# Performance work log

Measured on AMD Instinct MI355X. Metric: run time of the kernel, lower is better.

Reference implementation:

```python
import jax, jax.numpy as jnp
import numpy as np

N, E, F, C, H, DK, CV, RH, B, OUT = 50000, 800000, 32, 64, 4, 32, 16, 16, 128, 64


def setup_inputs() -> dict:
    key = jax.random.key(0)
    ks = jax.random.split(key, 16)
    s = lambda k, shape, fan: jax.random.normal(k, shape, jnp.float32) / np.float32(np.sqrt(fan))
    return {
        'pos': jax.random.normal(ks[0], (N, 3), jnp.float32),
        'node_features': jax.random.normal(ks[1], (N, F), jnp.float32),
        'edge_index': jax.random.randint(ks[2], (2, E), 0, N),
        'batch': jnp.sort(jax.random.randint(ks[3], (N,), 0, B)),
        'W_emb': s(ks[4], (F, C), F), 'b_emb': jnp.zeros((C,), jnp.float32),
        'Wq': s(ks[5], (H, C, DK), C), 'Wk': s(ks[6], (H, C, DK), C),
        'Wv0': s(ks[7], (H, C, CV), C), 'Wv1': s(ks[8], (H, C, CV), C),
        'R1': s(ks[9], (H, 1, RH), 1), 'b1': jnp.zeros((H, RH), jnp.float32),
        'R2': s(ks[10], (H, RH, DK + 2 * CV), RH), 'b2': jnp.zeros((H, DK + 2 * CV), jnp.float32),
        'Wproj': s(ks[11], (H * CV, OUT), H * CV),
    }


def reference(pos, node_features, edge_index, batch, W_emb, b_emb, Wq, Wk, Wv0, Wv1, R1, b1, R2, b2, Wproj):
    src, dst = edge_index[0], edge_index[1]
    # relative positions, distances, normalized directions (= l=1 spherical harmonics)
    rel = pos[dst] - pos[src]                       # [E,3]
    d = jnp.linalg.norm(rel, axis=-1, keepdims=True) + 1e-8  # [E,1]
    Y1 = rel / d                                    # l=1 SH (unit direction); l=0 SH is constant
    # initial scalar embedding (torch.nn.Linear)
    h = node_features @ W_emb + b_emb               # [N,C]
    hs = h[src]                                     # [E,C] edge gather
    # per-head queries / radially-modulated keys
    q = jnp.einsum('nc,hck->hnk', h, Wq)            # [H,N,DK]
    ksrc = jnp.einsum('ec,hck->hek', hs, Wk)        # [H,E,DK]
    rh = jax.nn.silu(jnp.einsum('ei,hir->her', d, R1) + b1[:, None, :])  # radial MLP [H,E,RH]
    rout = jnp.einsum('her,hro->heo', rh, R2) + b2[:, None, :]           # [H,E,DK+2CV]
    rk, rv0, rv1 = rout[..., :DK], rout[..., DK:DK + CV], rout[..., DK + CV:]
    ke = ksrc * rk
    scores = jnp.einsum('hek,hek->he', q[:, dst], ke).T / np.float32(np.sqrt(DK))  # [E,H]
    # segment softmax over incoming edges of each destination node
    m = jax.ops.segment_max(scores, dst, num_segments=N)   # [N,H]
    ex = jnp.exp(scores - m[dst])
    denom = jax.ops.segment_sum(ex, dst, num_segments=N)
    alpha = ex / (denom[dst] + 1e-9)                       # [E,H]
    # equivariant values: scalar (0e) and vector (1o = scalar coeff * Y1) channels
    v0 = jnp.einsum('ec,hcv->ehv', hs, Wv0) * rv0.transpose(1, 0, 2)   # [E,H,CV]
    c1 = jnp.einsum('ec,hcv->ehv', hs, Wv1) * rv1.transpose(1, 0, 2)   # [E,H,CV]
    vec = c1[..., None] * Y1[:, None, None, :]                          # [E,H,CV,3]
    out0 = jax.ops.segment_sum(alpha[..., None] * v0, dst, num_segments=N)                       # [N,H,CV]
    out1 = jax.ops.segment_sum((alpha[..., None, None] * vec).reshape(E, H, CV * 3), dst, num_segments=N)  # [N,H,3CV]
    feat = jnp.concatenate([out0, out1], axis=-1)          # [N,H,4CV] per-head 16x0e+16x1o, concat over heads
    # global_add_pool by graph id
    pooled = jax.ops.segment_sum(feat, batch, num_segments=B)  # [B,H,4CV]
    # irrep-aware projection to 64x0e: only 0e channels contribute
    scal = pooled[:, :, :CV].reshape(B, H * CV)
    return scal @ Wproj
```

## Files before the change

### kernel.cpp

```cpp
#include <hip/hip_runtime.h>
#include <hip/hip_fp16.h>

static inline int idiv_up(long a, long b) { return (int)((a + b - 1) / b); }

#define RADIAL_G 2048
#define GBASE    (119 << 7)
#define MAXDEG   64

typedef _Float16 h2 __attribute__((ext_vector_type(2)));

__device__ __forceinline__ unsigned pack_h2(float a, float b) {
    __half2 t = __floats2half2_rn(a, b);
    return *reinterpret_cast<unsigned*>(&t);
}
__device__ __forceinline__ unsigned pack_h1(float a) {
    __half t = __float2half_rn(a);
    return (unsigned)*reinterpret_cast<unsigned short*>(&t);
}
__device__ __forceinline__ h2 as_h2(unsigned u) {
    return *reinterpret_cast<h2*>(&u);
}
__device__ __forceinline__ _Float16 as_h1(unsigned u) {
    unsigned short s = (unsigned short)u;
    return *reinterpret_cast<_Float16*>(&s);
}
__device__ __forceinline__ float dot2(h2 a, h2 b) {
#if __has_builtin(__builtin_amdgcn_fdot2)
    return __builtin_amdgcn_fdot2(a, b, 0.f, false);
#else
    return (float)a.x * (float)b.x + (float)a.y * (float)b.y;
#endif
}

template <int CTRL>
__device__ __forceinline__ float dppf(float x) {
    return __int_as_float(__builtin_amdgcn_update_dpp(
        0, __float_as_int(x), CTRL, 0xF, 0xF, true));
}
__device__ __forceinline__ float row_allsum(float p) {
    p += dppf<0xB1>(p);
    p += dppf<0x4E>(p);
    p += dppf<0x124>(p);
    p += dppf<0x128>(p);
    return p;
}

#define FOLD_B 42
__global__ __launch_bounds__(256) void fold_tab(
    const float* __restrict__ W_emb, const float* __restrict__ b_emb,
    const float* __restrict__ Wq, const float* __restrict__ Wk,
    const float* __restrict__ Wv0,
    float* __restrict__ Wcomb, float* __restrict__ bcomb,
    const float* __restrict__ R1, const float* __restrict__ b1,
    const float* __restrict__ R2, const float* __restrict__ b2,
    unsigned* __restrict__ TAB)
{
    if (blockIdx.x < FOLD_B) {
        int idx = blockIdx.x * 256 + threadIdx.x;
        if (idx >= 33 * 320) return;
        int row = idx / 320, j = idx - row * 320;
        float acc = 0.f;
        for (int c = 0; c < 64; ++c) {
            float w;
            if (j < 128)      { int h = j >> 5,         k = j & 31;         w = Wq [(h * 64 + c) * 32 + k]; }
            else if (j < 256) { int h = (j - 128) >> 5, k = (j - 128) & 31; w = Wk [(h * 64 + c) * 32 + k]; }
            else              { int h = (j - 256) >> 4, v = (j - 256) & 15; w = Wv0[(h * 64 + c) * 16 + v]; }
            float lhs = (row < 32) ? W_emb[row * 64 + c] : b_emb[c];
            acc += lhs * w;
        }
        if (row < 32) Wcomb[row * 320 + j] = acc;
        else          bcomb[j] = acc;
        return;
    }
    {
        int idx = ((int)blockIdx.x - FOLD_B) * 256 + threadIdx.x;
        if (idx >= RADIAL_G * 64) return;
        int g = idx >> 6, lane = idx & 63;
        int h = lane >> 4, j = lane & 15;
        float d = __uint_as_float(((unsigned)(g + GBASE) << 16) | 0x8000u);
        float rh[16];
#pragma unroll
        for (int r = 0; r < 16; ++r) {
            float x = fmaf(d, R1[h * 16 + r], b1[h * 16 + r]);
            rh[r] = x / (1.f + __expf(-x));
        }
        float rk0 = b2[h * 64 + j], rk1 = b2[h * 64 + j + 16], rv = b2[h * 64 + 32 + j];
#pragma unroll
        for (int r = 0; r < 16; ++r) {
            const float* row = R2 + (size_t)(h * 16 + r) * 64;
            rk0 = fmaf(rh[r], row[j], rk0);
            rk1 = fmaf(rh[r], row[j + 16], rk1);
            rv  = fmaf(rh[r], row[32 + j], rv);
        }
        const float rs = 0.17677669529663687f * 1.4426950408889634f;
        TAB[(size_t)g * 128 + 2 * lane]     = pack_h2(rk0 * rs, rk1 * rs);
        TAB[(size_t)g * 128 + 2 * lane + 1] = pack_h1(rv);
    }
}

__global__ __launch_bounds__(256) void qkv_scatter(
    const float* __restrict__ nf, const float* __restrict__ Wcomb,
    const float* __restrict__ bcomb, unsigned* __restrict__ Qt,
    unsigned* __restrict__ KVt,
    const float* __restrict__ pos, const int* __restrict__ ei,
    int* __restrict__ cursor, unsigned* __restrict__ csrp,
    int Nn, int Ee, int edge2B)
{
    if ((int)blockIdx.x < edge2B) {
        int base = (int)blockIdx.x * 512 + threadIdx.x;
        int e0 = base, e1 = base + 256;
        bool v0 = e0 < Ee, v1 = e1 < Ee;
        int s0 = 0, d0 = 0, s1 = 0, d1 = 0;
        if (v0) { s0 = ei[e0]; d0 = ei[Ee + e0]; }
        if (v1) { s1 = ei[e1]; d1 = ei[Ee + e1]; }
        float dd0 = 0.f, dd1 = 0.f;
        if (v0) {
            float dx = pos[(size_t)d0 * 3 + 0] - pos[(size_t)s0 * 3 + 0];
            float dy = pos[(size_t)d0 * 3 + 1] - pos[(size_t)s0 * 3 + 1];
            float dz = pos[(size_t)d0 * 3 + 2] - pos[(size_t)s0 * 3 + 2];
            dd0 = sqrtf(dx * dx + dy * dy + dz * dz) + 1e-8f;
        }
        if (v1) {
            float dx = pos[(size_t)d1 * 3 + 0] - pos[(size_t)s1 * 3 + 0];
            float dy = pos[(size_t)d1 * 3 + 1] - pos[(size_t)s1 * 3 + 1];
            float dz = pos[(size_t)d1 * 3 + 2] - pos[(size_t)s1 * 3 + 2];
            dd1 = sqrtf(dx * dx + dy * dy + dz * dz) + 1e-8f;
        }
        if (v0) {
            int g = (__float_as_int(dd0) >> 16) - GBASE;
            g = min(max(g, 0), RADIAL_G - 1);
            int r = atomicAdd(&cursor[d0], 1);
            if (r < MAXDEG)
                csrp[((size_t)d0 << 6) + r] = (unsigned)s0 | ((unsigned)g << 20);
        }
        if (v1) {
            int g = (__float_as_int(dd1) >> 16) - GBASE;
            g = min(max(g, 0), RADIAL_G - 1);
            int r = atomicAdd(&cursor[d1], 1);
            if (r < MAXDEG)
                csrp[((size_t)d1 << 6) + r] = (unsigned)s1 | ((unsigned)g << 20);
        }
        return;
    }
    int bx   = (int)blockIdx.x - edge2B;
    int c    = bx % 10;
    int tile = bx / 10;
    int n = tile * 256 + threadIdx.x;
    bool valid = n < Nn;
    int nc = valid ? n : (Nn - 1);

    float nfv[32];
    const float4* nfp = (const float4*)(nf + (size_t)nc * 32);
#pragma unroll
    for (int f4 = 0; f4 < 8; ++f4) {
        float4 v = nfp[f4];
        nfv[f4 * 4 + 0] = v.x; nfv[f4 * 4 + 1] = v.y;
        nfv[f4 * 4 + 2] = v.z; nfv[f4 * 4 + 3] = v.w;
    }
    const float* Wc = Wcomb + c * 32;
    float acc[32];
#pragma unroll
    for (int j4 = 0; j4 < 8; ++j4) {
        float4 b = *(const float4*)&bcomb[c * 32 + j4 * 4];
        acc[j4 * 4 + 0] = b.x; acc[j4 * 4 + 1] = b.y;
        acc[j4 * 4 + 2] = b.z; acc[j4 * 4 + 3] = b.w;
    }
#pragma unroll
    for (int f = 0; f < 32; ++f) {
        float x = nfv[f];
        const float* row = Wc + f * 320;
#pragma unroll
        for (int j4 = 0; j4 < 8; ++j4) {
            float4 w = *(const float4*)&row[j4 * 4];
            acc[j4 * 4 + 0] = fmaf(x, w.x, acc[j4 * 4 + 0]);
            acc[j4 * 4 + 1] = fmaf(x, w.y, acc[j4 * 4 + 1]);
            acc[j4 * 4 + 2] = fmaf(x, w.z, acc[j4 * 4 + 2]);
            acc[j4 * 4 + 3] = fmaf(x, w.w, acc[j4 * 4 + 3]);
        }
    }
    if (!valid) return;
    if (c < 4) {
        unsigned* qp = Qt + (size_t)n * 64 + c * 16;
#pragma unroll
        for (int jj = 0; jj < 16; ++jj)
            qp[jj] = pack_h2(acc[jj], acc[jj + 16]);
    } else if (c < 8) {
        unsigned* kp = KVt + ((size_t)n << 7) + (c - 4) * 16;
#pragma unroll
        for (int jj = 0; jj < 16; ++jj)
            kp[jj] = pack_h2(acc[jj], acc[jj + 16]);
    } else {
        unsigned short* vp = (unsigned short*)(KVt + ((size_t)n << 7) + 64) + (c - 8) * 32;
#pragma unroll
        for (int jj = 0; jj < 32; ++jj)
            vp[jj] = (unsigned short)pack_h1(acc[jj]);
    }
}

__global__ __launch_bounds__(256) void calc_hist(
    const int* __restrict__ cursor, int* __restrict__ ghist, int Nn)
{
    __shared__ int lh[128];
    if (threadIdx.x < 128) lh[threadIdx.x] = 0;
    __syncthreads();
    int n = blockIdx.x * 256 + threadIdx.x;
    if (n < Nn) {
        int d = min(cursor[n], MAXDEG);
        atomicAdd(&lh[d], 1);
    }
    __syncthreads();
    if (threadIdx.x < 128 && lh[threadIdx.x])
        atomicAdd(&ghist[threadIdx.x], lh[threadIdx.x]);
}

__global__ __launch_bounds__(128) void bin_scan(
    const int* __restrict__ ghist, int* __restrict__ bcur)
{
    __shared__ int s[128];
    s[threadIdx.x] = ghist[threadIdx.x];
    __syncthreads();
    int sum = 0;
    for (int b = threadIdx.x + 1; b < 128; ++b) sum += s[b];
    bcur[threadIdx.x] = sum;
}

__global__ __launch_bounds__(256) void perm_scatter(
    const int* __restrict__ cursor, int* __restrict__ bcur,
    int* __restrict__ perm, int Nn)
{
    __shared__ int lh[128], lbase[128];
    if (threadIdx.x < 128) lh[threadIdx.x] = 0;
    __syncthreads();
    int n = blockIdx.x * 256 + threadIdx.x;
    int bk = -1, r = 0;
    if (n < Nn) {
        bk = min(cursor[n], MAXDEG);
        r = atomicAdd(&lh[bk], 1);
    }
    __syncthreads();
    if (threadIdx.x < 128 && lh[threadIdx.x])
        lbase[threadIdx.x] = atomicAdd(&bcur[threadIdx.x], lh[threadIdx.x]);
    __syncthreads();
    if (n < Nn) perm[lbase[bk] + r] = n;
}

struct Pair {
    unsigned ku0, vu0, ku1, vu1;
    uint2 tb0, tb1;
};

__global__ __launch_bounds__(128) void node_attn(
    const unsigned* __restrict__ Qt, const unsigned* __restrict__ KVt,
    const uint2* __restrict__ TAB, const unsigned* __restrict__ csrp,
    const int* __restrict__ cursor, const int* __restrict__ batch,
    const int* __restrict__ perm, float* __restrict__ pooled, int Nn)
{
    int lane = threadIdx.x & 63;
    int wv = blockIdx.x * 2 + (threadIdx.x >> 6);
    if (wv >= Nn) return;
    int n = perm[wv];
    int cnt = min(cursor[n], MAXDEG);
    if (cnt == 0) return;
    int start = n << 6;

    h2 qh = as_h2(Qt[(size_t)n * 64 + lane]);
    float l = 0.f, acc = 0.f;

    auto LD1 = [&](int ei, unsigned& ku, unsigned& vu, uint2& tb) {
        unsigned pk = csrp[ei];
        unsigned src = pk & 0xFFFFFu;
        unsigned g   = pk >> 20;
        tb = TAB[((size_t)g << 6) + lane];
        const unsigned* kb = KVt + ((size_t)src << 7);
        ku = kb[lane];
        vu = (unsigned)((const unsigned short*)(kb + 64))[lane];
    };
    auto LDP = [&](Pair& P, int ei) {
        LD1(ei,     P.ku0, P.vu0, P.tb0);
        LD1(ei + 1, P.ku1, P.vu1, P.tb1);
    };
    auto CMP1 = [&](unsigned ku, unsigned vu, uint2 tb) {
        h2 prod = as_h2(ku) * as_h2(tb.x);
        float p = dot2(qh, prod);
        p = row_allsum(p);
        float ex = exp2f(fminf(p, 110.f));
        l += ex;
        float w = (float)(as_h1(vu) * as_h1(tb.y));
        acc = fmaf(ex, w, acc);
    };
    auto CMP = [&](const Pair& P) {
        CMP1(P.ku0, P.vu0, P.tb0);
        CMP1(P.ku1, P.vu1, P.tb1);
    };

    int e = start, end = start + cnt;
    Pair A, B, C;
    if (e + 5 < end) {
        LDP(A, e); LDP(B, e + 2); LDP(C, e + 4);
        for (; e + 11 < end; e += 6) {
            CMP(A); LDP(A, e + 6);
            CMP(B); LDP(B, e + 8);
            CMP(C); LDP(C, e + 10);
        }
        CMP(A); CMP(B); CMP(C);
        e += 6;
    }
    for (; e + 1 < end; e += 2) { LDP(A, e); CMP(A); }
    if (e < end) {
        unsigned ku, vu; uint2 tb;
        LD1(e, ku, vu, tb);
        CMP1(ku, vu, tb);
    }
    float o = acc / (l + 1e-30f);
    atomicAdd(&pooled[(size_t)batch[n] * 64 + lane], o);
}

__global__ __launch_bounds__(256) void final_proj(
    const float* __restrict__ pooled, const float* __restrict__ Wproj,
    float* __restrict__ out, int total)
{
    int idx = blockIdx.x * 256 + threadIdx.x;
    if (idx >= total) return;
    int b = idx >> 6, o = idx & 63;
    float acc = 0.f;
#pragma unroll
    for (int i = 0; i < 64; ++i) acc += pooled[b * 64 + i] * Wproj[i * 64 + o];
    out[idx] = acc;
}

extern "C" void kernel_launch(void* const* d_in, const int* in_sizes, int n_in,
                              void* d_out, int out_size, void* d_ws, size_t ws_size,
                              hipStream_t stream)
{
    const float* pos   = (const float*)d_in[0];
    const float* nf    = (const float*)d_in[1];
    const int*   ei    = (const int*)d_in[2];
    const int*   batch = (const int*)d_in[3];
    const float* W_emb = (const float*)d_in[4];
    const float* b_emb = (const float*)d_in[5];
    const float* Wq    = (const float*)d_in[6];
    const float* Wk    = (const float*)d_in[7];
    const float* Wv0   = (const float*)d_in[8];
    const float* R1    = (const float*)d_in[10];
    const float* b1    = (const float*)d_in[11];
    const float* R2    = (const float*)d_in[12];
    const float* b2    = (const float*)d_in[13];
    const float* Wproj = (const float*)d_in[14];
    float* out = (float*)d_out;

    long Nn = in_sizes[0] / 3;
    long Ee = in_sizes[2] / 2;
    int  Bb = out_size / 64;

    float* ws = (float*)d_ws;
    size_t o = 0;
    size_t WCOMB = o; o += 32 * 320;
    size_t BCOMB = o; o += 320;
    size_t QTAB  = o; o += (size_t)Nn * 64;
    size_t KVT   = o; o += (size_t)Nn * 128;
    size_t CURS  = o; o += (size_t)Nn;
    size_t GHIST = o; o += 128;
    size_t POOL  = o; o += (size_t)Bb * 64;
    size_t BCUR  = o; o += 128;
    size_t PERM  = o; o += (size_t)Nn;
    size_t CSR   = o; o += (size_t)Nn * MAXDEG;
    o = (o + 1) & ~(size_t)1;
    size_t TAB   = o; o += (size_t)RADIAL_G * 128;

    hipMemsetAsync(ws + CURS, 0,
                   ((size_t)Nn + 128 + (size_t)Bb * 64) * sizeof(float), stream);

    int edge2B = idiv_up(Ee, 512);
    int nodeB  = idiv_up(Nn, 256);
    int tabB   = idiv_up(RADIAL_G * 64, 256);
    int qkvB   = nodeB * 10;

    fold_tab<<<FOLD_B + tabB, 256, 0, stream>>>(
        W_emb, b_emb, Wq, Wk, Wv0, ws + WCOMB, ws + BCOMB,
        R1, b1, R2, b2, (unsigned*)(ws + TAB));

    qkv_scatter<<<edge2B + qkvB, 256, 0, stream>>>(
        nf, ws + WCOMB, ws + BCOMB, (unsigned*)(ws + QTAB),
        (unsigned*)(ws + KVT), pos, ei,
        (int*)(ws + CURS), (unsigned*)(ws + CSR), (int)Nn, (int)Ee, edge2B);

    calc_hist<<<nodeB, 256, 0, stream>>>(
        (const int*)(ws + CURS), (int*)(ws + GHIST), (int)Nn);

    bin_scan<<<1, 128, 0, stream>>>(
        (const int*)(ws + GHIST), (int*)(ws + BCUR));

    perm_scatter<<<nodeB, 256, 0, stream>>>(
        (const int*)(ws + CURS), (int*)(ws + BCUR), (int*)(ws + PERM), (int)Nn);

    node_attn<<<idiv_up(Nn, 2), 128, 0, stream>>>(
        (const unsigned*)(ws + QTAB), (const unsigned*)(ws + KVT),
        (const uint2*)(ws + TAB), (const unsigned*)(ws + CSR),
        (const int*)(ws + CURS), batch, (const int*)(ws + PERM),
        ws + POOL, (int)Nn);

    final_proj<<<idiv_up(out_size, 256), 256, 0, stream>>>(
        ws + POOL, Wproj, out, out_size);
}
```

Baseline: 162.5 us.

## Drop degree-sorted node permutation and pad positions to float4

Removes the three-kernel degree histogram, scan and permutation pipeline so the attention kernel processes nodes in natural order. This eliminates three launches and a permutation gather, at the cost of losing degree-balanced scheduling across wavefronts. Positions are also repacked into a float4 array in the fold kernel so each edge does one vector load per endpoint instead of three scalar loads.

```diff
diff --git a/kernel.cpp b/kernel.cpp
--- a/kernel.cpp
+++ b/kernel.cpp
@@ -46,14 +46,16 @@
 }
 
 #define FOLD_B 42
-__global__ __launch_bounds__(256) void fold_tab(
+__global__ __launch_bounds__(256) void fold_tab_pos(
     const float* __restrict__ W_emb, const float* __restrict__ b_emb,
     const float* __restrict__ Wq, const float* __restrict__ Wk,
     const float* __restrict__ Wv0,
     float* __restrict__ Wcomb, float* __restrict__ bcomb,
     const float* __restrict__ R1, const float* __restrict__ b1,
     const float* __restrict__ R2, const float* __restrict__ b2,
-    unsigned* __restrict__ TAB)
+    unsigned* __restrict__ TAB,
+    const float* __restrict__ pos, float4* __restrict__ pos4,
+    int Nn, int tabB)
 {
     if (blockIdx.x < FOLD_B) {
         int idx = blockIdx.x * 256 + threadIdx.x;
@@ -72,8 +74,9 @@
         else          bcomb[j] = acc;
         return;
     }
-    {
-        int idx = ((int)blockIdx.x - FOLD_B) * 256 + threadIdx.x;
+    int bx = (int)blockIdx.x - FOLD_B;
+    if (bx < tabB) {
+        int idx = bx * 256 + threadIdx.x;
         if (idx >= RADIAL_G * 64) return;
         int g = idx >> 6, lane = idx & 63;
         int h = lane >> 4, j = lane & 15;
@@ -95,6 +98,18 @@
         const float rs = 0.17677669529663687f * 1.4426950408889634f;
         TAB[(size_t)g * 128 + 2 * lane]     = pack_h2(rk0 * rs, rk1 * rs);
         TAB[(size_t)g * 128 + 2 * lane + 1] = pack_h1(rv);
+        return;
+    }
+    bx -= tabB;
+    {
+        int n = bx * 256 + threadIdx.x;
+        if (n >= Nn) return;
+        float4 v;
+        v.x = pos[(size_t)n * 3 + 0];
+        v.y = pos[(size_t)n * 3 + 1];
+        v.z = pos[(size_t)n * 3 + 2];
+        v.w = 0.f;
+        pos4[n] = v;
     }
 }
 
@@ -102,7 +117,7 @@
     const float* __restrict__ nf, const float* __restrict__ Wcomb,
     const float* __restrict__ bcomb, unsigned* __restrict__ Qt,
     unsigned* __restrict__ KVt,
-    const float* __restrict__ pos, const int* __restrict__ ei,
+    const float4* __restrict__ pos4, const int* __restrict__ ei,
     int* __restrict__ cursor, unsigned* __restrict__ csrp,
     int Nn, int Ee, int edge2B)
 {
@@ -115,15 +130,13 @@
         if (v1) { s1 = ei[e1]; d1 = ei[Ee + e1]; }
         float dd0 = 0.f, dd1 = 0.f;
         if (v0) {
-            float dx = pos[(size_t)d0 * 3 + 0] - pos[(size_t)s0 * 3 + 0];
-            float dy = pos[(size_t)d0 * 3 + 1] - pos[(size_t)s0 * 3 + 1];
-            float dz = pos[(size_t)d0 * 3 + 2] - pos[(size_t)s0 * 3 + 2];
+            float4 a = pos4[d0], b = pos4[s0];
+            float dx = a.x - b.x, dy = a.y - b.y, dz = a.z - b.z;
             dd0 = sqrtf(dx * dx + dy * dy + dz * dz) + 1e-8f;
         }
         if (v1) {
-            float dx = pos[(size_t)d1 * 3 + 0] - pos[(size_t)s1 * 3 + 0];
-            float dy = pos[(size_t)d1 * 3 + 1] - pos[(size_t)s1 * 3 + 1];
-            float dz = pos[(size_t)d1 * 3 + 2] - pos[(size_t)s1 * 3 + 2];
+            float4 a = pos4[d1], b = pos4[s1];
+            float dx = a.x - b.x, dy = a.y - b.y, dz = a.z - b.z;
             dd1 = sqrtf(dx * dx + dy * dy + dz * dz) + 1e-8f;
         }
         if (v0) {
@@ -197,53 +210,6 @@
     }
 }
 
-__global__ __launch_bounds__(256) void calc_hist(
-    const int* __restrict__ cursor, int* __restrict__ ghist, int Nn)
-{
-    __shared__ int lh[128];
-    if (threadIdx.x < 128) lh[threadIdx.x] = 0;
-    __syncthreads();
-    int n = blockIdx.x * 256 + threadIdx.x;
-    if (n < Nn) {
-        int d = min(cursor[n], MAXDEG);
-        atomicAdd(&lh[d], 1);
-    }
-    __syncthreads();
-    if (threadIdx.x < 128 && lh[threadIdx.x])
-        atomicAdd(&ghist[threadIdx.x], lh[threadIdx.x]);
-}
-
-__global__ __launch_bounds__(128) void bin_scan(
-    const int* __restrict__ ghist, int* __restrict__ bcur)
-{
-    __shared__ int s[128];
-    s[threadIdx.x] = ghist[threadIdx.x];
-    __syncthreads();
-    int sum = 0;
-    for (int b = threadIdx.x + 1; b < 128; ++b) sum += s[b];
-    bcur[threadIdx.x] = sum;
-}
-
-__global__ __launch_bounds__(256) void perm_scatter(
-    const int* __restrict__ cursor, int* __restrict__ bcur,
-    int* __restrict__ perm, int Nn)
-{
-    __shared__ int lh[128], lbase[128];
-    if (threadIdx.x < 128) lh[threadIdx.x] = 0;
-    __syncthreads();
-    int n = blockIdx.x * 256 + threadIdx.x;
-    int bk = -1, r = 0;
-    if (n < Nn) {
-        bk = min(cursor[n], MAXDEG);
-        r = atomicAdd(&lh[bk], 1);
-    }
-    __syncthreads();
-    if (threadIdx.x < 128 && lh[threadIdx.x])
-        lbase[threadIdx.x] = atomicAdd(&bcur[threadIdx.x], lh[threadIdx.x]);
-    __syncthreads();
-    if (n < Nn) perm[lbase[bk] + r] = n;
-}
-
 struct Pair {
     unsigned ku0, vu0, ku1, vu1;
     uint2 tb0, tb1;
@@ -253,12 +219,11 @@
     const unsigned* __restrict__ Qt, const unsigned* __restrict__ KVt,
     const uint2* __restrict__ TAB, const unsigned* __restrict__ csrp,
     const int* __restrict__ cursor, const int* __restrict__ batch,
-    const int* __restrict__ perm, float* __restrict__ pooled, int Nn)
+    float* __restrict__ pooled, int Nn)
 {
     int lane = threadIdx.x & 63;
-    int wv = blockIdx.x * 2 + (threadIdx.x >> 6);
-    if (wv >= Nn) return;
-    int n = perm[wv];
+    int n = blockIdx.x * 2 + (threadIdx.x >> 6);
+    if (n >= Nn) return;
     int cnt = min(cursor[n], MAXDEG);
     if (cnt == 0) return;
     int start = n << 6;
@@ -359,45 +324,34 @@
     size_t QTAB  = o; o += (size_t)Nn * 64;
     size_t KVT   = o; o += (size_t)Nn * 128;
     size_t CURS  = o; o += (size_t)Nn;
-    size_t GHIST = o; o += 128;
     size_t POOL  = o; o += (size_t)Bb * 64;
-    size_t BCUR  = o; o += 128;
-    size_t PERM  = o; o += (size_t)Nn;
     size_t CSR   = o; o += (size_t)Nn * MAXDEG;
-    o = (o + 1) & ~(size_t)1;
+    o = (o + 3) & ~(size_t)3;
+    size_t POS4  = o; o += (size_t)Nn * 4;
     size_t TAB   = o; o += (size_t)RADIAL_G * 128;
 
     hipMemsetAsync(ws + CURS, 0,
-                   ((size_t)Nn + 128 + (size_t)Bb * 64) * sizeof(float), stream);
+                   ((size_t)Nn + (size_t)Bb * 64) * sizeof(float), stream);
 
     int edge2B = idiv_up(Ee, 512);
     int nodeB  = idiv_up(Nn, 256);
     int tabB   = idiv_up(RADIAL_G * 64, 256);
     int qkvB   = nodeB * 10;
 
-    fold_tab<<<FOLD_B + tabB, 256, 0, stream>>>(
+    fold_tab_pos<<<FOLD_B + tabB + nodeB, 256, 0, stream>>>(
         W_emb, b_emb, Wq, Wk, Wv0, ws + WCOMB, ws + BCOMB,
-        R1, b1, R2, b2, (unsigned*)(ws + TAB));
+        R1, b1, R2, b2, (unsigned*)(ws + TAB),
+        pos, (float4*)(ws + POS4), (int)Nn, tabB);
 
     qkv_scatter<<<edge2B + qkvB, 256, 0, stream>>>(
         nf, ws + WCOMB, ws + BCOMB, (unsigned*)(ws + QTAB),
-        (unsigned*)(ws + KVT), pos, ei,
+        (unsigned*)(ws + KVT), (const float4*)(ws + POS4), ei,
         (int*)(ws + CURS), (unsigned*)(ws + CSR), (int)Nn, (int)Ee, edge2B);
-
-    calc_hist<<<nodeB, 256, 0, stream>>>(
-        (const int*)(ws + CURS), (int*)(ws + GHIST), (int)Nn);
-
-    bin_scan<<<1, 128, 0, stream>>>(
-        (const int*)(ws + GHIST), (int*)(ws + BCUR));
-
-    perm_scatter<<<nodeB, 256, 0, stream>>>(
-        (const int*)(ws + CURS), (int*)(ws + BCUR), (int*)(ws + PERM), (int)Nn);
 
     node_attn<<<idiv_up(Nn, 2), 128, 0, stream>>>(
         (const unsigned*)(ws + QTAB), (const unsigned*)(ws + KVT),
         (const uint2*)(ws + TAB), (const unsigned*)(ws + CSR),
-        (const int*)(ws + CURS), batch, (const int*)(ws + PERM),
-        ws + POOL, (int)Nn);
+        (const int*)(ws + CURS), batch, ws + POOL, (int)Nn);
 
     final_proj<<<idiv_up(out_size, 256), 256, 0, stream>>>(
         ws + POOL, Wproj, out, out_size);
```

Measured after the change: 174.6 us. 1.07x slower.
